# Kernel optimization log

Hardware: AMD Instinct MI355X
Metric: run time of the kernel (lower is better)

The kernel has to match this reference:

```python
import jax, jax.numpy as jnp
import numpy as np

B, L, H, E, F, C = 8, 8192, 512, 8, 1024, 2  # batch, seq, hidden, experts, ffn, capacity factor


def setup_inputs() -> dict:
    key = jax.random.key(0)
    ks = jax.random.split(key, 4)
    x = jax.random.normal(ks[0], (B, L, H), jnp.float32)
    Wg = jax.random.normal(ks[1], (H, E), jnp.float32) * (H ** -0.5)   # gate (no bias)
    W1 = jax.random.normal(ks[2], (E, H, F), jnp.float32) * (H ** -0.5)
    b1 = jnp.zeros((E, F), jnp.float32)
    W2 = jax.random.normal(ks[3], (E, F, H), jnp.float32) * (F ** -0.5)
    b2 = jnp.zeros((E, H), jnp.float32)
    return {"x": x, "Wg": Wg, "W1": W1, "b1": b1, "W2": W2, "b2": b2}


def reference(x, Wg, W1, b1, W2, b2):
    b, l, h = x.shape
    e = Wg.shape[1]
    k = min(max(int(l * C / e), 1), l)  # expert-choice capacity per expert
    # Gate scores: softmax over experts per token, then each expert picks its top-k tokens.
    S = jax.nn.softmax(x @ Wg, axis=-1)          # (b, l, E)
    St = jnp.swapaxes(S, 1, 2)                   # (b, E, l)
    G, I = jax.lax.top_k(St, k)                  # (b, E, k) scores / token indices
    # Dispatch: gather each expert's chosen tokens.
    ex = jnp.take_along_axis(x[:, None], I[..., None], axis=2)   # (b, E, k, h)
    # Grouped expert MLP (Linear -> GELU -> Linear), batched over experts.
    hmid = jax.nn.gelu(jnp.einsum('bekh,ehf->bekf', ex, W1) + b1[None, :, None, :],
                       approximate=False)
    out = jnp.einsum('bekf,efh->bekh', hmid, W2) + b2[None, :, None, :]
    vals = G[..., None] * out                    # weight by gate score
    # Combine: scatter-add expert outputs back to token positions.
    new_x = jnp.zeros_like(x).at[jnp.arange(b)[:, None, None], I].add(vals)
    return new_x
```

## Files before the change

kernel.cpp:

```cpp
#include <hip/hip_runtime.h>
#include <hip/hip_bf16.h>
#include <hip/hip_fp16.h>

typedef float f32x4 __attribute__((ext_vector_type(4)));
typedef _Float16 f16x8 __attribute__((ext_vector_type(8)));
typedef unsigned int u32x4 __attribute__((ext_vector_type(4)));

static constexpr int Bb = 8, Ll = 8192, Hh = 512, Ee = 8, Ff = 1024, KK = 2048;

static __device__ __forceinline__ float fast_rcp(float x) {
#if __has_builtin(__builtin_amdgcn_rcpf)
  return __builtin_amdgcn_rcpf(x);
#else
  return 1.0f / x;
#endif
}

static __device__ __forceinline__ float gelu_exact(float v) {
  float a = __builtin_fabsf(v) * 0.70710678118654752f;
  float t = fast_rcp(__builtin_fmaf(0.47047f, a, 1.0f));
  float p = __builtin_fmaf(0.7478556f, t, -0.0958798f);
  p = __builtin_fmaf(p, t, 0.3480242f);
  p = p * t;
  float e = __expf(-a * a);
  float er = __builtin_fmaf(-p, e, 1.0f);
  er = __builtin_copysignf(er, v);
  return 0.5f * v * (1.0f + er);
}

static __device__ __forceinline__ void nt_store16(const f16x8& v, _Float16* p) {
  __builtin_nontemporal_store(*reinterpret_cast<const u32x4*>(&v),
                              reinterpret_cast<u32x4*>(p));
}

__global__ __launch_bounds__(256) void transpose_cvt_kernel(const float* __restrict__ src,
                                                            _Float16* __restrict__ dst,
                                                            int R, int C) {
  __shared__ float tile[32][33];
  int z = blockIdx.z;
  const float* s = src + (size_t)z * R * C;
  _Float16* d = dst + (size_t)z * R * C;
  int c0 = blockIdx.x * 32, r0 = blockIdx.y * 32;
  int tx = threadIdx.x, ty = threadIdx.y;
#pragma unroll
  for (int i = ty; i < 32; i += 8) tile[i][tx] = s[(size_t)(r0 + i) * C + (c0 + tx)];
  __syncthreads();
#pragma unroll
  for (int i = ty; i < 32; i += 8) d[(size_t)(c0 + i) * R + (r0 + tx)] = (_Float16)tile[tx][i];
}

__global__ __launch_bounds__(256) void gatecvt_kernel(const float* __restrict__ x,
                                                      const float* __restrict__ Wg,
                                                      double* __restrict__ St,
                                                      _Float16* __restrict__ xb) {
  __shared__ float wgt[8][516];
  __shared__ float xs[32][132];
  int tid = threadIdx.x;
  for (int i = tid; i < Hh * Ee; i += 256) wgt[i & 7][i >> 3] = Wg[i];
  int row = tid >> 3, seg = tid & 7;
  int token0 = blockIdx.x * 32;
  const float* xrow = x + (size_t)(token0 + row) * Hh;
  _Float16* xbrow = xb + (size_t)(token0 + row) * Hh;
  float4 r0 = reinterpret_cast<const float4*>(xrow)[seg * 4 + 0];
  float4 r1 = reinterpret_cast<const float4*>(xrow)[seg * 4 + 1];
  float4 r2 = reinterpret_cast<const float4*>(xrow)[seg * 4 + 2];
  float4 r3 = reinterpret_cast<const float4*>(xrow)[seg * 4 + 3];
  double a0 = 0.0, a1 = 0.0, a2 = 0.0, a3 = 0.0;
  for (int c = 0; c < 4; ++c) {
    f16x8 h0, h1;
    h0[0] = (_Float16)r0.x; h0[1] = (_Float16)r0.y; h0[2] = (_Float16)r0.z; h0[3] = (_Float16)r0.w;
    h0[4] = (_Float16)r1.x; h0[5] = (_Float16)r1.y; h0[6] = (_Float16)r1.z; h0[7] = (_Float16)r1.w;
    h1[0] = (_Float16)r2.x; h1[1] = (_Float16)r2.y; h1[2] = (_Float16)r2.z; h1[3] = (_Float16)r2.w;
    h1[4] = (_Float16)r3.x; h1[5] = (_Float16)r3.y; h1[6] = (_Float16)r3.z; h1[7] = (_Float16)r3.w;
    nt_store16(h0, xbrow + c * 128 + seg * 16);
    nt_store16(h1, xbrow + c * 128 + seg * 16 + 8);
    __syncthreads();
    *reinterpret_cast<float4*>(&xs[row][seg * 16 + 0]) = r0;
    *reinterpret_cast<float4*>(&xs[row][seg * 16 + 4]) = r1;
    *reinterpret_cast<float4*>(&xs[row][seg * 16 + 8]) = r2;
    *reinterpret_cast<float4*>(&xs[row][seg * 16 + 12]) = r3;
    if (c + 1 < 4) {
      const float4* nx = reinterpret_cast<const float4*>(xrow + (c + 1) * 128);
      r0 = nx[seg * 4 + 0]; r1 = nx[seg * 4 + 1]; r2 = nx[seg * 4 + 2]; r3 = nx[seg * 4 + 3];
    }
    __syncthreads();
#pragma unroll
    for (int hh = 0; hh < 128; hh += 4) {
      float4 xv = *reinterpret_cast<const float4*>(&xs[row][hh]);
      float4 wv = *reinterpret_cast<const float4*>(&wgt[seg][c * 128 + hh]);
      a0 += (double)xv.x * (double)wv.x;
      a1 += (double)xv.y * (double)wv.y;
      a2 += (double)xv.z * (double)wv.z;
      a3 += (double)xv.w * (double)wv.w;
    }
  }
  double acc = (a0 + a1) + (a2 + a3);
  double m = acc;
  m = fmax(m, __shfl_xor(m, 1, 64));
  m = fmax(m, __shfl_xor(m, 2, 64));
  m = fmax(m, __shfl_xor(m, 4, 64));
  double ex = exp(acc - m);
  double s = ex;
  s += __shfl_xor(s, 1, 64);
  s += __shfl_xor(s, 2, 64);
  s += __shfl_xor(s, 4, 64);
  int token = token0 + row;
  int b = token >> 13, l = token & (Ll - 1);
  St[((size_t)(b * Ee + seg)) * Ll + l] = ex / s;
}

__global__ __launch_bounds__(1024) void topk_kernel(const double* __restrict__ St,
                                                    int* __restrict__ idx,
                                                    float* __restrict__ gate) {
  __shared__ unsigned long long keys[Ll];
  __shared__ unsigned int hist[256];
  __shared__ unsigned int sc[1024];
  __shared__ unsigned long long s_prefix;
  __shared__ int s_remaining;
  __shared__ unsigned long long redA[16], redO[16];
  int row = blockIdx.x;
  int tid = threadIdx.x;
  const double* s = St + (size_t)row * Ll;
  unsigned long long myA = ~0ULL, myO = 0ULL;
  for (int i = tid; i < Ll; i += 1024) {
    unsigned long long kx = (unsigned long long)__double_as_longlong(s[i]);
    keys[i] = kx;
    myA &= kx;
    myO |= kx;
  }
#pragma unroll
  for (int off2 = 32; off2 >= 1; off2 >>= 1) {
    myA &= __shfl_xor(myA, off2, 64);
    myO |= __shfl_xor(myO, off2, 64);
  }
  if ((tid & 63) == 0) { redA[tid >> 6] = myA; redO[tid >> 6] = myO; }
  __syncthreads();
  unsigned long long allA = redA[0], allO = redO[0];
#pragma unroll
  for (int w = 1; w < 16; ++w) { allA &= redA[w]; allO |= redO[w]; }
  unsigned long long diff = allA ^ allO;

  unsigned long long T;
  int nEqTake;
  if (diff == 0) {
    T = allA;
    nEqTake = KK;
  } else {
    int hb = 63 - __builtin_clzll(diff);
    int pv = hb >> 3;
    unsigned long long prefmask = (pv >= 7) ? 0ULL : (~0ULL << ((pv + 1) * 8));
    unsigned long long prefix = allA & prefmask;
    int remaining = KK;
    for (int p = pv; p >= 0; --p) {
      if (tid < 256) hist[tid] = 0;
      __syncthreads();
      int sh = p * 8;
      for (int i = tid; i < Ll; i += 1024) {
        unsigned long long kk = keys[i];
        if ((kk & prefmask) == prefix) atomicAdd(&hist[(unsigned)(kk >> sh) & 255u], 1u);
      }
      __syncthreads();
      if (tid < 256) sc[tid] = hist[tid];
      __syncthreads();
#pragma unroll
      for (int off = 1; off < 256; off <<= 1) {
        unsigned v = (tid < 256 && tid + off < 256) ? sc[tid + off] : 0;
        __syncthreads();
        if (tid < 256) sc[tid] += v;
        __syncthreads();
      }
      if (tid < 256) {
        unsigned incl = sc[tid];
        unsigned above = (tid == 255) ? 0u : sc[tid + 1];
        if ((int)incl >= remaining && (int)above < remaining) {
          s_remaining = remaining - (int)above;
          s_prefix = prefix | ((unsigned long long)(unsigned)tid << sh);
        }
      }
      __syncthreads();
      remaining = s_remaining;
      prefix = s_prefix;
      prefmask |= (255ULL << sh);
      __syncthreads();
    }
    T = prefix;
    nEqTake = remaining;
  }

  int base = tid * 8;
  unsigned long long kk[8];
  unsigned gtc = 0, eqc = 0;
#pragma unroll
  for (int j = 0; j < 8; ++j) {
    kk[j] = keys[base + j];
    gtc += (kk[j] > T);
    eqc += (kk[j] == T);
  }
  unsigned packed = (gtc << 16) | eqc;
  sc[tid] = packed;
  __syncthreads();
  for (int off = 1; off < 1024; off <<= 1) {
    unsigned v = (tid >= off) ? sc[tid - off] : 0;
    __syncthreads();
    sc[tid] += v;
    __syncthreads();
  }
  unsigned excl = sc[tid] - packed;
  int gtb = (int)(excl >> 16), eqb = (int)(excl & 0xFFFFu);
  int orow = row * KK;
#pragma unroll
  for (int j = 0; j < 8; ++j) {
    bool isgt = kk[j] > T, iseq = kk[j] == T;
    bool take = isgt || (iseq && eqb < nEqTake);
    if (take) {
      int pos = gtb + (eqb < nEqTake ? eqb : nEqTake);
      idx[orow + pos] = base + j;
      gate[orow + pos] = (float)__longlong_as_double((long long)kk[j]);
    }
    gtb += isgt ? 1 : 0;
    eqb += iseq ? 1 : 0;
  }
}

__global__ __launch_bounds__(256) void buildinv_kernel(const int* __restrict__ idx,
                                                       int* __restrict__ cnt,
                                                       int* __restrict__ inv) {
  int s = blockIdx.x * 256 + threadIdx.x;
  int gp = s >> 11;
  int b = gp >> 3;
  int t = idx[s];
  int key = b * Ll + t;
  int pos = atomicAdd(&cnt[key], 1);
  inv[key * 8 + pos] = s;
}

__global__ __launch_bounds__(256) void combine_kernel(const _Float16* __restrict__ yout,
                                                      const int* __restrict__ cnt,
                                                      const int* __restrict__ inv,
                                                      float* __restrict__ out) {
  int tglob = blockIdx.x * 4 + (threadIdx.x >> 6);
  int lane = threadIdx.x & 63;
  int n = cnt[tglob];
  float acc[8];
#pragma unroll
  for (int j = 0; j < 8; ++j) acc[j] = 0.f;
  for (int c = 0; c < n; ++c) {
    int s = inv[tglob * 8 + c];
    u32x4 u = __builtin_nontemporal_load(
        reinterpret_cast<const u32x4*>(yout + (size_t)s * Hh + lane * 8));
    f16x8 v = *reinterpret_cast<f16x8*>(&u);
#pragma unroll
    for (int j = 0; j < 8; ++j) acc[j] += (float)v[j];
  }
  float* o = out + (size_t)tglob * Hh + lane * 8;
  f32x4 lo = {acc[0], acc[1], acc[2], acc[3]};
  f32x4 hi = {acc[4], acc[5], acc[6], acc[7]};
  __builtin_nontemporal_store(lo, reinterpret_cast<f32x4*>(o));
  __builtin_nontemporal_store(hi, reinterpret_cast<f32x4*>(o + 4));
}

__global__ __launch_bounds__(512, 2) void gemm1_kernel(const _Float16* __restrict__ xb,
                                                       const _Float16* __restrict__ w1t,
                                                       const float* __restrict__ b1,
                                                       const int* __restrict__ idx,
                                                       _Float16* __restrict__ hmid,
                                                       int chunk_base) {
  __shared__ __align__(16) _Float16 lds[65536];
  int tid = threadIdx.x, lane = tid & 63, wid = tid >> 6;
  int nat = blockIdx.x;
  int rr = nat >> 8;
  int j = nat & 7;
  int idxb = (nat >> 3) & 31;
  int pl = rr * 8 + j;
  int bx = idxb & 3, by = idxb >> 2;
  int gp = chunk_base + pl;
  int b = gp >> 3, e = gp & 7;
  int m0 = by * 256, f0 = bx * 256;

  const _Float16* srcbase[8];
  int dstoff[8];
#pragma unroll
  for (int i = 0; i < 8; ++i) {
    int c = wid * 8 + i;
    int lr = (c & 31) * 8 + (lane >> 3);
    int q = lane & 7;
    int qg = q ^ (lr & 7);
    if (c < 32) {
      int token = idx[(size_t)gp * KK + m0 + lr];
      srcbase[i] = xb + ((size_t)b * Ll + token) * Hh + qg * 8;
      dstoff[i] = (c & 31) * 512;
    } else {
      srcbase[i] = w1t + ((size_t)e * Ff + f0 + lr) * Hh + qg * 8;
      dstoff[i] = 16384 + (c & 31) * 512;
    }
  }

  f32x4 acc[8][4] = {};
  int wm = wid >> 2, wn = wid & 3;
  int a_off[8], b_off[4];
  int ko = lane >> 4;
#pragma unroll
  for (int i = 0; i < 8; ++i) {
    int ra = wm * 128 + i * 16 + (lane & 15);
    a_off[i] = ra * 64 + (ko ^ (ra & 7)) * 8;
  }
#pragma unroll
  for (int i = 0; i < 4; ++i) {
    int rb = wn * 64 + i * 16 + (lane & 15);
    b_off[i] = 16384 + rb * 64 + (ko ^ (rb & 7)) * 8;
  }

  auto stage = [&](int p, int kt) {
#pragma unroll
    for (int i = 0; i < 8; ++i) {
      __builtin_amdgcn_global_load_lds(
          (const __attribute__((address_space(1))) void*)(srcbase[i] + kt),
          (__attribute__((address_space(3))) void*)(lds + p * 32768 + dstoff[i]), 16, 0, 0);
    }
  };

  constexpr int nt = Hh / 64;
  stage(0, 0);
  for (int t = 0; t < nt; ++t) {
    __syncthreads();
    if (t + 1 < nt) stage((t + 1) & 1, (t + 1) * 64);
    const _Float16* buf = lds + (t & 1) * 32768;
#pragma unroll
    for (int half = 0; half < 2; ++half) {
      int kx = half * 32;
      f16x8 af[8], bf[4];
#pragma unroll
      for (int i = 0; i < 8; ++i) af[i] = *reinterpret_cast<const f16x8*>(buf + (a_off[i] ^ kx));
#pragma unroll
      for (int i = 0; i < 4; ++i) bf[i] = *reinterpret_cast<const f16x8*>(buf + (b_off[i] ^ kx));
      __builtin_amdgcn_s_setprio(1);
#pragma unroll
      for (int fr = 0; fr < 8; ++fr)
#pragma unroll
        for (int fc = 0; fc < 4; ++fc)
          acc[fr][fc] = __builtin_amdgcn_mfma_f32_16x16x32_f16(af[fr], bf[fc], acc[fr][fc], 0, 0, 0);
      __builtin_amdgcn_s_setprio(0);
    }
  }
  __syncthreads();

  int cidx = lane & 15, rbase = (lane >> 4) * 4;
  float b1v[4];
#pragma unroll
  for (int fc = 0; fc < 4; ++fc) b1v[fc] = b1[e * Ff + f0 + wn * 64 + fc * 16 + cidx];
#pragma unroll
  for (int fr = 0; fr < 8; ++fr) {
#pragma unroll
    for (int fc = 0; fc < 4; ++fc) {
#pragma unroll
      for (int r = 0; r < 4; ++r) {
        int lm = wm * 128 + fr * 16 + rbase + r;
        int lf = wn * 64 + fc * 16 + cidx;
        float v = acc[fr][fc][r] + b1v[fc];
        lds[lm * 256 + (((lf >> 3) ^ (lm & 7)) << 3) + (lf & 7)] = (_Float16)gelu_exact(v);
      }
    }
  }
  __syncthreads();
  _Float16* hd = hmid + (size_t)pl * KK * Ff;
  int orow = tid >> 5, seg = tid & 31;
#pragma unroll
  for (int pp = 0; pp < 16; ++pp) {
    int lm = pp * 16 + orow;
    f16x8 v = *reinterpret_cast<const f16x8*>(lds + lm * 256 + ((seg ^ (lm & 7)) << 3));
    nt_store16(v, hd + (size_t)(m0 + lm) * Ff + f0 + seg * 8);
  }
}

__global__ __launch_bounds__(512, 2) void gemm2_kernel(const _Float16* __restrict__ hmid,
                                                       const _Float16* __restrict__ w2t,
                                                       const float* __restrict__ b2,
                                                       const int* __restrict__ idx,
                                                       const float* __restrict__ gate,
                                                       _Float16* __restrict__ yout,
                                                       int chunk_base, int small8) {
  __shared__ __align__(16) _Float16 lds[65536];
  int tid = threadIdx.x, lane = tid & 63, wid = tid >> 6;
  int nat = blockIdx.x;
  int ci, by;
  if (small8) {
    int j = nat & 7;
    int idxb = nat >> 3;
    ci = j * 2 + (idxb >> 3);
    by = idxb & 7;
  } else {
    int rr = nat >> 8;
    int low = nat & 255;
    int j = low & 7;
    int idxb = low >> 3;
    ci = rr * 32 + j * 4 + (idxb >> 3);
    by = idxb & 7;
  }
  int pl = ci >> 1;
  int h0 = (ci & 1) * 256;
  int gp = chunk_base + pl;
  int e = gp & 7;
  int m0 = by * 256;

  const _Float16* srcbase[8];
  int dstoff[8];
#pragma unroll
  for (int i = 0; i < 8; ++i) {
    int c = wid * 8 + i;
    int lr = (c & 31) * 8 + (lane >> 3);
    int q = lane & 7;
    int qg = q ^ (lr & 7);
    if (c < 32) {
      srcbase[i] = hmid + ((size_t)pl * KK + m0 + lr) * Ff + qg * 8;
      dstoff[i] = (c & 31) * 512;
    } else {
      srcbase[i] = w2t + ((size_t)e * Hh + h0 + lr) * Ff + qg * 8;
      dstoff[i] = 16384 + (c & 31) * 512;
    }
  }

  f32x4 acc[8][4] = {};
  int wm = wid >> 2, wn = wid & 3;
  int a_off[8], b_off[4];
  int ko = lane >> 4;
#pragma unroll
  for (int i = 0; i < 8; ++i) {
    int ra = wm * 128 + i * 16 + (lane & 15);
    a_off[i] = ra * 64 + (ko ^ (ra & 7)) * 8;
  }
#pragma unroll
  for (int i = 0; i < 4; ++i) {
    int rb = wn * 64 + i * 16 + (lane & 15);
    b_off[i] = 16384 + rb * 64 + (ko ^ (rb & 7)) * 8;
  }

  auto stage = [&](int p, int kt) {
#pragma unroll
    for (int i = 0; i < 8; ++i) {
      __builtin_amdgcn_global_load_lds(
          (const __attribute__((address_space(1))) void*)(srcbase[i] + kt),
          (__attribute__((address_space(3))) void*)(lds + p * 32768 + dstoff[i]), 16, 0, 0);
    }
  };

  constexpr int nt = Ff / 64;
  stage(0, 0);
  for (int t = 0; t < nt; ++t) {
    __syncthreads();
    if (t + 1 < nt) stage((t + 1) & 1, (t + 1) * 64);
    const _Float16* buf = lds + (t & 1) * 32768;
#pragma unroll
    for (int half = 0; half < 2; ++half) {
      int kx = half * 32;
      f16x8 af[8], bf[4];
#pragma unroll
      for (int i = 0; i < 8; ++i) af[i] = *reinterpret_cast<const f16x8*>(buf + (a_off[i] ^ kx));
#pragma unroll
      for (int i = 0; i < 4; ++i) bf[i] = *reinterpret_cast<const f16x8*>(buf + (b_off[i] ^ kx));
      __builtin_amdgcn_s_setprio(1);
#pragma unroll
      for (int fr = 0; fr < 8; ++fr)
#pragma unroll
        for (int fc = 0; fc < 4; ++fc)
          acc[fr][fc] = __builtin_amdgcn_mfma_f32_16x16x32_f16(af[fr], bf[fc], acc[fr][fc], 0, 0, 0);
      __builtin_amdgcn_s_setprio(0);
    }
  }
  __syncthreads();

  int cidx = lane & 15, rbase = (lane >> 4) * 4;
  float b2v[4];
#pragma unroll
  for (int fc = 0; fc < 4; ++fc) b2v[fc] = b2[e * Hh + h0 + wn * 64 + fc * 16 + cidx];
#pragma unroll
  for (int fr = 0; fr < 8; ++fr) {
    float gv[4];
#pragma unroll
    for (int r = 0; r < 4; ++r) {
      int lm = wm * 128 + fr * 16 + rbase + r;
      gv[r] = gate[(size_t)gp * KK + m0 + lm];
    }
#pragma unroll
    for (int fc = 0; fc < 4; ++fc) {
#pragma unroll
      for (int r = 0; r < 4; ++r) {
        int lm = wm * 128 + fr * 16 + rbase + r;
        int lh = wn * 64 + fc * 16 + cidx;
        float v = acc[fr][fc][r] + b2v[fc];
        lds[lm * 256 + (((lh >> 3) ^ (lm & 7)) << 3) + (lh & 7)] = (_Float16)(gv[r] * v);
      }
    }
  }
  __syncthreads();
  int orow = tid >> 5, seg = tid & 31;
#pragma unroll
  for (int pp = 0; pp < 16; ++pp) {
    int lm = pp * 16 + orow;
    f16x8 v = *reinterpret_cast<const f16x8*>(lds + lm * 256 + ((seg ^ (lm & 7)) << 3));
    nt_store16(v, yout + ((size_t)gp * KK + m0 + lm) * Hh + h0 + seg * 8);
  }
}

extern "C" void kernel_launch(void* const* d_in, const int* in_sizes, int n_in,
                              void* d_out, int out_size, void* d_ws, size_t ws_size,
                              hipStream_t stream) {
  const float* x  = (const float*)d_in[0];
  const float* Wg = (const float*)d_in[1];
  const float* W1 = (const float*)d_in[2];
  const float* b1 = (const float*)d_in[3];
  const float* W2 = (const float*)d_in[4];
  const float* b2 = (const float*)d_in[5];
  float* out = (float*)d_out;

  char* ws = (char*)d_ws;
  size_t off = 0;
  auto alloc = [&](size_t bytes) -> char* {
    char* p = ws + off;
    off = (off + bytes + 255) & ~(size_t)255;
    return p;
  };
  _Float16* xb   = (_Float16*)alloc((size_t)Bb * Ll * Hh * 2);
  _Float16* w1t  = (_Float16*)alloc((size_t)Ee * Ff * Hh * 2);
  _Float16* w2t  = (_Float16*)alloc((size_t)Ee * Hh * Ff * 2);
  double*   St   = (double*)alloc((size_t)Bb * Ee * Ll * 8);
  int*      dI   = (int*)alloc((size_t)Bb * Ee * KK * 4);
  float*    dG   = (float*)alloc((size_t)Bb * Ee * KK * 4);
  int*      cnt  = (int*)alloc((size_t)Bb * Ll * 4);
  int*      inv  = (int*)alloc((size_t)Bb * Ll * 8 * 4);
  _Float16* yout = (_Float16*)alloc((size_t)Bb * Ee * KK * Hh * 2);
  size_t fixed = off;
  size_t per_pair = (size_t)KK * Ff * 2;
  int chunk = 8;
  if (fixed + per_pair * 32 <= ws_size) chunk = 32;
  else if (fixed + per_pair * 16 <= ws_size) chunk = 16;
  _Float16* hmid = (_Float16*)alloc(per_pair * (size_t)chunk);

  hipMemsetAsync(cnt, 0, (size_t)Bb * Ll * 4, stream);
  gatecvt_kernel<<<Bb * Ll / 32, 256, 0, stream>>>(x, Wg, St, xb);
  transpose_cvt_kernel<<<dim3(Ff / 32, Hh / 32, Ee), dim3(32, 8), 0, stream>>>(W1, w1t, Hh, Ff);
  transpose_cvt_kernel<<<dim3(Hh / 32, Ff / 32, Ee), dim3(32, 8), 0, stream>>>(W2, w2t, Ff, Hh);
  topk_kernel<<<Bb * Ee, 1024, 0, stream>>>(St, dI, dG);
  buildinv_kernel<<<Bb * Ee * KK / 256, 256, 0, stream>>>(dI, cnt, inv);

  for (int cb = 0; cb < Bb * Ee; cb += chunk) {
    gemm1_kernel<<<chunk * 32, 512, 0, stream>>>(xb, w1t, b1, dI, hmid, cb);
    gemm2_kernel<<<chunk * 16, 512, 0, stream>>>(hmid, w2t, b2, dI, dG, yout, cb,
                                                 chunk == 8 ? 1 : 0);
  }
  combine_kernel<<<Bb * Ll / 4, 256, 0, stream>>>(yout, cnt, inv, out);
}
```

Measured before the change: 523.1 us.

## Make gemm1 persistent over expert pairs and overlap next prologue with epilogue

gemm1 now launches a fixed grid of 256 blocks, and each block loops over several (batch, expert) pairs. The first K-tile of the next pair is staged into the freed half of LDS while the GELU epilogue runs out of the other half, split into two 128-row passes. gemm1's hmid stores become regular rather than nontemporal, and the chunk size is capped at 16, which means more kernel launches. This aims to hide pipeline startup and epilogue time and to keep hmid resident in cache for gemm2, at the cost of less parallelism per launch and extra barriers.

After: 1.087 ms. 108% more time.

```diff
diff --git a/kernel.cpp b/kernel.cpp
--- a/kernel.cpp
+++ b/kernel.cpp
@@ -31,6 +31,13 @@
 static __device__ __forceinline__ void nt_store16(const f16x8& v, _Float16* p) {
   __builtin_nontemporal_store(*reinterpret_cast<const u32x4*>(&v),
                               reinterpret_cast<u32x4*>(p));
+}
+
+static __device__ __forceinline__ void lds_barrier() {
+  __builtin_amdgcn_sched_barrier(0);
+  asm volatile("s_waitcnt lgkmcnt(0)" ::: "memory");
+  __builtin_amdgcn_s_barrier();
+  __builtin_amdgcn_sched_barrier(0);
 }
 
 __global__ __launch_bounds__(256) void transpose_cvt_kernel(const float* __restrict__ src,
@@ -264,38 +271,14 @@
                                                        const float* __restrict__ b1,
                                                        const int* __restrict__ idx,
                                                        _Float16* __restrict__ hmid,
-                                                       int chunk_base) {
+                                                       int chunk_base, int nrounds) {
   __shared__ __align__(16) _Float16 lds[65536];
   int tid = threadIdx.x, lane = tid & 63, wid = tid >> 6;
-  int nat = blockIdx.x;
-  int rr = nat >> 8;
-  int j = nat & 7;
-  int idxb = (nat >> 3) & 31;
-  int pl = rr * 8 + j;
+  int j = blockIdx.x & 7;
+  int idxb = blockIdx.x >> 3;
   int bx = idxb & 3, by = idxb >> 2;
-  int gp = chunk_base + pl;
-  int b = gp >> 3, e = gp & 7;
   int m0 = by * 256, f0 = bx * 256;
 
-  const _Float16* srcbase[8];
-  int dstoff[8];
-#pragma unroll
-  for (int i = 0; i < 8; ++i) {
-    int c = wid * 8 + i;
-    int lr = (c & 31) * 8 + (lane >> 3);
-    int q = lane & 7;
-    int qg = q ^ (lr & 7);
-    if (c < 32) {
-      int token = idx[(size_t)gp * KK + m0 + lr];
-      srcbase[i] = xb + ((size_t)b * Ll + token) * Hh + qg * 8;
-      dstoff[i] = (c & 31) * 512;
-    } else {
-      srcbase[i] = w1t + ((size_t)e * Ff + f0 + lr) * Hh + qg * 8;
-      dstoff[i] = 16384 + (c & 31) * 512;
-    }
-  }
-
-  f32x4 acc[8][4] = {};
   int wm = wid >> 2, wn = wid & 3;
   int a_off[8], b_off[4];
   int ko = lane >> 4;
@@ -310,6 +293,31 @@
     b_off[i] = 16384 + rb * 64 + (ko ^ (rb & 7)) * 8;
   }
 
+  int sc_c[8], sc_lr[8], sc_qg[8];
+#pragma unroll
+  for (int i = 0; i < 8; ++i) {
+    int c = wid * 8 + i;
+    sc_c[i] = c;
+    sc_lr[i] = (c & 31) * 8 + (lane >> 3);
+    sc_qg[i] = (lane & 7) ^ (sc_lr[i] & 7);
+  }
+
+  const _Float16* srcbase[8];
+  int dstoff[8];
+  auto make_src = [&](int gp) {
+    int b = gp >> 3, e = gp & 7;
+#pragma unroll
+    for (int i = 0; i < 8; ++i) {
+      if (sc_c[i] < 32) {
+        int token = idx[(size_t)gp * KK + m0 + sc_lr[i]];
+        srcbase[i] = xb + ((size_t)b * Ll + token) * Hh + sc_qg[i] * 8;
+        dstoff[i] = sc_c[i] * 512;
+      } else {
+        srcbase[i] = w1t + ((size_t)e * Ff + f0 + sc_lr[i]) * Hh + sc_qg[i] * 8;
+        dstoff[i] = 16384 + (sc_c[i] & 31) * 512;
+      }
+    }
+  };
   auto stage = [&](int p, int kt) {
 #pragma unroll
     for (int i = 0; i < 8; ++i) {
@@ -319,56 +327,77 @@
     }
   };
 
-  constexpr int nt = Hh / 64;
+  make_src(chunk_base + j);
   stage(0, 0);
-  for (int t = 0; t < nt; ++t) {
+
+  for (int rr = 0; rr < nrounds; ++rr) {
+    int pl = rr * 8 + j;
+    int gp = chunk_base + pl;
+    int e = gp & 7;
+
+    f32x4 acc[8][4] = {};
+    constexpr int nt = Hh / 64;
+    for (int t = 0; t < nt; ++t) {
+      __syncthreads();
+      if (t + 1 < nt) stage((t + 1) & 1, (t + 1) * 64);
+      const _Float16* buf = lds + (t & 1) * 32768;
+#pragma unroll
+      for (int half = 0; half < 2; ++half) {
+        int kx = half * 32;
+        f16x8 af[8], bf[4];
+#pragma unroll
+        for (int i = 0; i < 8; ++i) af[i] = *reinterpret_cast<const f16x8*>(buf + (a_off[i] ^ kx));
+#pragma unroll
+        for (int i = 0; i < 4; ++i) bf[i] = *reinterpret_cast<const f16x8*>(buf + (b_off[i] ^ kx));
+        __builtin_amdgcn_s_setprio(1);
+#pragma unroll
+        for (int fr = 0; fr < 8; ++fr)
+#pragma unroll
+          for (int fc = 0; fc < 4; ++fc)
+            acc[fr][fc] = __builtin_amdgcn_mfma_f32_16x16x32_f16(af[fr], bf[fc], acc[fr][fc], 0, 0, 0);
+        __builtin_amdgcn_s_setprio(0);
+      }
+    }
     __syncthreads();
-    if (t + 1 < nt) stage((t + 1) & 1, (t + 1) * 64);
-    const _Float16* buf = lds + (t & 1) * 32768;
-#pragma unroll
-    for (int half = 0; half < 2; ++half) {
-      int kx = half * 32;
-      f16x8 af[8], bf[4];
-#pragma unroll
-      for (int i = 0; i < 8; ++i) af[i] = *reinterpret_cast<const f16x8*>(buf + (a_off[i] ^ kx));
-#pragma unroll
-      for (int i = 0; i < 4; ++i) bf[i] = *reinterpret_cast<const f16x8*>(buf + (b_off[i] ^ kx));
-      __builtin_amdgcn_s_setprio(1);
-#pragma unroll
-      for (int fr = 0; fr < 8; ++fr)
-#pragma unroll
-        for (int fc = 0; fc < 4; ++fc)
-          acc[fr][fc] = __builtin_amdgcn_mfma_f32_16x16x32_f16(af[fr], bf[fc], acc[fr][fc], 0, 0, 0);
-      __builtin_amdgcn_s_setprio(0);
-    }
-  }
-  __syncthreads();
-
-  int cidx = lane & 15, rbase = (lane >> 4) * 4;
-  float b1v[4];
-#pragma unroll
-  for (int fc = 0; fc < 4; ++fc) b1v[fc] = b1[e * Ff + f0 + wn * 64 + fc * 16 + cidx];
-#pragma unroll
-  for (int fr = 0; fr < 8; ++fr) {
-#pragma unroll
-    for (int fc = 0; fc < 4; ++fc) {
-#pragma unroll
-      for (int r = 0; r < 4; ++r) {
-        int lm = wm * 128 + fr * 16 + rbase + r;
-        int lf = wn * 64 + fc * 16 + cidx;
-        float v = acc[fr][fc][r] + b1v[fc];
-        lds[lm * 256 + (((lf >> 3) ^ (lm & 7)) << 3) + (lf & 7)] = (_Float16)gelu_exact(v);
-      }
-    }
-  }
-  __syncthreads();
-  _Float16* hd = hmid + (size_t)pl * KK * Ff;
-  int orow = tid >> 5, seg = tid & 31;
-#pragma unroll
-  for (int pp = 0; pp < 16; ++pp) {
-    int lm = pp * 16 + orow;
-    f16x8 v = *reinterpret_cast<const f16x8*>(lds + lm * 256 + ((seg ^ (lm & 7)) << 3));
-    nt_store16(v, hd + (size_t)(m0 + lm) * Ff + f0 + seg * 8);
+
+    if (rr + 1 < nrounds) {
+      make_src(gp + 8);
+      stage(0, 0);
+    }
+
+    _Float16* ep = lds + 32768;
+    _Float16* hd = hmid + (size_t)pl * KK * Ff;
+    int cidx = lane & 15, rbase = (lane >> 4) * 4;
+    float b1v[4];
+#pragma unroll
+    for (int fc = 0; fc < 4; ++fc) b1v[fc] = b1[e * Ff + f0 + wn * 64 + fc * 16 + cidx];
+#pragma unroll
+    for (int pass = 0; pass < 2; ++pass) {
+      if (wm == pass) {
+#pragma unroll
+        for (int fr = 0; fr < 8; ++fr) {
+#pragma unroll
+          for (int fc = 0; fc < 4; ++fc) {
+#pragma unroll
+            for (int r = 0; r < 4; ++r) {
+              int rl = fr * 16 + rbase + r;
+              int lf = wn * 64 + fc * 16 + cidx;
+              float v = acc[fr][fc][r] + b1v[fc];
+              ep[rl * 256 + (((lf >> 3) ^ (rl & 7)) << 3) + (lf & 7)] = (_Float16)gelu_exact(v);
+            }
+          }
+        }
+      }
+      lds_barrier();
+      int orow = tid >> 5, seg = tid & 31;
+#pragma unroll
+      for (int pp = 0; pp < 8; ++pp) {
+        int rl = pp * 16 + orow;
+        f16x8 v = *reinterpret_cast<const f16x8*>(ep + rl * 256 + ((seg ^ (rl & 7)) << 3));
+        *reinterpret_cast<f16x8*>(hd + (size_t)(m0 + pass * 128 + rl) * Ff + f0 + seg * 8) = v;
+      }
+      lds_barrier();
+    }
   }
 }
 
@@ -389,11 +418,9 @@
     ci = j * 2 + (idxb >> 3);
     by = idxb & 7;
   } else {
-    int rr = nat >> 8;
-    int low = nat & 255;
-    int j = low & 7;
-    int idxb = low >> 3;
-    ci = rr * 32 + j * 4 + (idxb >> 3);
+    int j = nat & 7;
+    int idxb = nat >> 3;
+    ci = j * 4 + (idxb >> 3);
     by = idxb & 7;
   }
   int pl = ci >> 1;
@@ -468,36 +495,43 @@
   }
   __syncthreads();
 
+  _Float16* ep = lds + 32768;
   int cidx = lane & 15, rbase = (lane >> 4) * 4;
   float b2v[4];
 #pragma unroll
   for (int fc = 0; fc < 4; ++fc) b2v[fc] = b2[e * Hh + h0 + wn * 64 + fc * 16 + cidx];
 #pragma unroll
-  for (int fr = 0; fr < 8; ++fr) {
-    float gv[4];
-#pragma unroll
-    for (int r = 0; r < 4; ++r) {
-      int lm = wm * 128 + fr * 16 + rbase + r;
-      gv[r] = gate[(size_t)gp * KK + m0 + lm];
-    }
-#pragma unroll
-    for (int fc = 0; fc < 4; ++fc) {
-#pragma unroll
-      for (int r = 0; r < 4; ++r) {
-        int lm = wm * 128 + fr * 16 + rbase + r;
-        int lh = wn * 64 + fc * 16 + cidx;
-        float v = acc[fr][fc][r] + b2v[fc];
-        lds[lm * 256 + (((lh >> 3) ^ (lm & 7)) << 3) + (lh & 7)] = (_Float16)(gv[r] * v);
-      }
-    }
-  }
-  __syncthreads();
-  int orow = tid >> 5, seg = tid & 31;
-#pragma unroll
-  for (int pp = 0; pp < 16; ++pp) {
-    int lm = pp * 16 + orow;
-    f16x8 v = *reinterpret_cast<const f16x8*>(lds + lm * 256 + ((seg ^ (lm & 7)) << 3));
-    nt_store16(v, yout + ((size_t)gp * KK + m0 + lm) * Hh + h0 + seg * 8);
+  for (int pass = 0; pass < 2; ++pass) {
+    if (wm == pass) {
+#pragma unroll
+      for (int fr = 0; fr < 8; ++fr) {
+        float gv[4];
+#pragma unroll
+        for (int r = 0; r < 4; ++r) {
+          int lm = pass * 128 + fr * 16 + rbase + r;
+          gv[r] = gate[(size_t)gp * KK + m0 + lm];
+        }
+#pragma unroll
+        for (int fc = 0; fc < 4; ++fc) {
+#pragma unroll
+          for (int r = 0; r < 4; ++r) {
+            int rl = fr * 16 + rbase + r;
+            int lh = wn * 64 + fc * 16 + cidx;
+            float v = acc[fr][fc][r] + b2v[fc];
+            ep[rl * 256 + (((lh >> 3) ^ (rl & 7)) << 3) + (lh & 7)] = (_Float16)(gv[r] * v);
+          }
+        }
+      }
+    }
+    lds_barrier();
+    int orow = tid >> 5, seg = tid & 31;
+#pragma unroll
+    for (int pp = 0; pp < 8; ++pp) {
+      int rl = pp * 16 + orow;
+      f16x8 v = *reinterpret_cast<const f16x8*>(ep + rl * 256 + ((seg ^ (rl & 7)) << 3));
+      nt_store16(v, yout + ((size_t)gp * KK + m0 + pass * 128 + rl) * Hh + h0 + seg * 8);
+    }
+    lds_barrier();
   }
 }
 
@@ -530,9 +564,7 @@
   _Float16* yout = (_Float16*)alloc((size_t)Bb * Ee * KK * Hh * 2);
   size_t fixed = off;
   size_t per_pair = (size_t)KK * Ff * 2;
-  int chunk = 8;
-  if (fixed + per_pair * 32 <= ws_size) chunk = 32;
-  else if (fixed + per_pair * 16 <= ws_size) chunk = 16;
+  int chunk = (fixed + per_pair * 16 <= ws_size) ? 16 : 8;
   _Float16* hmid = (_Float16*)alloc(per_pair * (size_t)chunk);
 
   hipMemsetAsync(cnt, 0, (size_t)Bb * Ll * 4, stream);
@@ -543,7 +575,7 @@
   buildinv_kernel<<<Bb * Ee * KK / 256, 256, 0, stream>>>(dI, cnt, inv);
 
   for (int cb = 0; cb < Bb * Ee; cb += chunk) {
-    gemm1_kernel<<<chunk * 32, 512, 0, stream>>>(xb, w1t, b1, dI, hmid, cb);
+    gemm1_kernel<<<256, 512, 0, stream>>>(xb, w1t, b1, dI, hmid, cb, chunk / 8);
     gemm2_kernel<<<chunk * 16, 512, 0, stream>>>(hmid, w2t, b2, dI, dG, yout, cb,
                                                  chunk == 8 ? 1 : 0);
   }
```
